# Kernel optimization log

Hardware: AMD Instinct MI355X
Metric: run time of the kernel (lower is better)

The kernel has to match this reference:

```python
import jax, jax.numpy as jnp
import numpy as np

LN_EPS = 1e-5  # torch.nn.LayerNorm default


def setup_inputs() -> dict:
    key = jax.random.key(0)
    k1, k2, k3 = jax.random.split(key, 3)
    B, N, F, D = 8, 2048, 128, 128
    A_hat = jax.random.uniform(k1, (B, N, N), dtype=jnp.float32)
    X = jax.random.normal(k2, (B, N, F), dtype=jnp.float32)
    W = jax.random.normal(k3, (D, F), dtype=jnp.float32) * (1.0 / np.sqrt(F))
    b = jnp.zeros((D,), dtype=jnp.float32)
    gamma = jnp.ones((D,), dtype=jnp.float32)
    beta = jnp.zeros((D,), dtype=jnp.float32)
    return {"A_hat": A_hat, "X": X, "W": W, "b": b, "gamma": gamma, "beta": beta}


def reference(A_hat, X, W, b, gamma, beta):
    # batched aggregation: H[b] = A_hat[b] @ X[b]   (torch loop over batch, vectorized here)
    H = jnp.einsum('bnm,bmf->bnf', A_hat, X)
    # linear: torch nn.Linear stores W as [out, in]
    H = jnp.einsum('bnf,df->bnd', H, W) + b
    # LayerNorm over last dim, then ReLU (dropout p=0 -> identity)
    mu = jnp.mean(H, axis=-1, keepdims=True)
    var = jnp.mean((H - mu) ** 2, axis=-1, keepdims=True)
    Hn = (H - mu) * jax.lax.rsqrt(var + LN_EPS) * gamma + beta
    return jax.nn.relu(Hn)
```

## Files before the change

### kernel.cpp

```cpp
#include <hip/hip_runtime.h>
#include <stdint.h>

#define B_DIM 8
#define N_DIM 2048
#define F_DIM 128
#define LN_EPS 1e-5f

typedef __attribute__((ext_vector_type(8))) short short8;
typedef __attribute__((ext_vector_type(4))) float floatx4;

__device__ __forceinline__ ushort f2bf(float f) {
    union { float f; uint32_t u; } c;
    c.f = f;
    uint32_t u = c.u;
    return (ushort)((u + 0x7FFFu + ((u >> 16) & 1u)) >> 16);
}

__device__ __forceinline__ uint32_t pk2bf(float a, float b) {
    union { float f; uint32_t u; } x, y;
    x.f = a; y.f = b;
    return ((x.u + 0x8000u) >> 16) | ((y.u + 0x8000u) & 0xFFFF0000u);
}

__device__ __forceinline__ short8 pack8(float4 lo, float4 hi) {
    union { uint32_t u[4]; short8 s; } r;
    r.u[0] = pk2bf(lo.x, lo.y);
    r.u[1] = pk2bf(lo.z, lo.w);
    r.u[2] = pk2bf(hi.x, hi.y);
    r.u[3] = pk2bf(hi.z, hi.w);
    return r.s;
}

__device__ __forceinline__ void load_lds16(const ushort* g, ushort* l) {
    __builtin_amdgcn_global_load_lds(
        (const __attribute__((address_space(1))) void*)g,
        (__attribute__((address_space(3))) void*)l,
        16, 0, 0);
}

__global__ __launch_bounds__(256) void k_prep(const float* __restrict__ X,
                                              const float* __restrict__ W,
                                              ushort* __restrict__ Yt) {
    __shared__ __align__(16) ushort Xs[64 * 128];
    const int t = threadIdx.x;
    const int lane = t & 63;
    const int w = t >> 6;
    const int q = lane >> 4;
    const int mr = lane & 15;

    const int b = blockIdx.x >> 5;
    const int k0 = (blockIdx.x & 31) * 64;

    const int r = t >> 2;
    const int f0 = (t & 3) * 32;
    const float* src = X + (((size_t)b * N_DIM) + k0 + r) * F_DIM + f0;
    float4 v[8];
#pragma unroll
    for (int p = 0; p < 8; ++p) v[p] = ((const float4*)src)[p];
#pragma unroll
    for (int c2 = 0; c2 < 4; ++c2) {
        int chunk = (f0 >> 3) + c2;
        *(short8*)(Xs + r * 128 + ((chunk ^ (r & 7)) * 8)) =
            pack8(v[2 * c2], v[2 * c2 + 1]);
    }
    __syncthreads();

    floatx4 acc[4][2];
#pragma unroll
    for (int i = 0; i < 4; ++i)
#pragma unroll
        for (int j = 0; j < 2; ++j) acc[i][j] = (floatx4){0.f, 0.f, 0.f, 0.f};

#pragma unroll
    for (int ks = 0; ks < 4; ++ks) {
        short8 af[4];
#pragma unroll
        for (int i = 0; i < 4; ++i) {
            int m = i * 16 + mr;
            af[i] = *(const short8*)(Xs + m * 128 + (((ks * 4 + q) ^ (m & 7)) * 8));
        }
#pragma unroll
        for (int j = 0; j < 2; ++j) {
            const float* wp = W + (w * 32 + j * 16 + mr) * F_DIM + ks * 32 + q * 8;
            short8 wb = pack8(((const float4*)wp)[0], ((const float4*)wp)[1]);
#pragma unroll
            for (int i = 0; i < 4; ++i)
                acc[i][j] = __builtin_amdgcn_mfma_f32_16x16x32_bf16(af[i], wb,
                                                                    acc[i][j], 0, 0, 0);
        }
    }

#pragma unroll
    for (int i = 0; i < 4; ++i)
#pragma unroll
        for (int j = 0; j < 2; ++j) {
            int d = w * 32 + j * 16 + mr;
            union { ushort s[4]; uint2 u; } o;
#pragma unroll
            for (int r2 = 0; r2 < 4; ++r2) o.s[r2] = f2bf(acc[i][j][r2]);
            *(uint2*)(Yt + (((size_t)b * F_DIM) + d) * N_DIM + k0 + i * 16 + q * 4) =
                o.u;
        }
}

__global__ __launch_bounds__(256, 2) void k_fused(const float* __restrict__ A,
                                                  const ushort* __restrict__ Yt,
                                                  const float* __restrict__ bias,
                                                  const float* __restrict__ gamma,
                                                  const float* __restrict__ beta,
                                                  float* __restrict__ out) {
    __shared__ __align__(16) char smem[81920];
    ushort* const As0 = (ushort*)smem;
    ushort* const As1 = (ushort*)(smem + 8192);
    ushort* const Bs0 = (ushort*)(smem + 16384);
    ushort* const Bs1 = (ushort*)(smem + 16384 + 32768);
    float (*const Pt)[132] = (float(*)[132])smem;

    const int t = threadIdx.x;
    const int lane = t & 63;
    const int w = t >> 6;
    const int q = lane >> 4;
    const int mr = lane & 15;

    const int bid = blockIdx.x;
    const int bb = bid & 7;
    const int m0 = (bid >> 3) * 32;

    const float* Ab = A + ((size_t)bb * N_DIM + m0) * N_DIM;
    const ushort* Yb = Yt + (size_t)bb * F_DIM * N_DIM;

    const int arow = t >> 3;
    const int asw_ = arow & 7;
    const float* a_src = Ab + (size_t)arow * N_DIM + (t & 7) * 16;
    const int a_off0 = arow * 128 + ((((t & 7) * 2) ^ asw_) * 8);
    const int a_off1 = arow * 128 + ((((t & 7) * 2 + 1) ^ asw_) * 8);

    const ushort* b_src[8];
    int b_off[8];
#pragma unroll
    for (int p = 0; p < 8; ++p) {
        int c = p * 256 + t;
        int n = c >> 4;
        int kc = (c & 15) ^ (n & 7);
        b_src[p] = Yb + (size_t)n * N_DIM + kc * 8;
        b_off[p] = c * 8;
    }

    floatx4 acc[2][2];
#pragma unroll
    for (int i = 0; i < 2; ++i)
#pragma unroll
        for (int j = 0; j < 2; ++j) acc[i][j] = (floatx4){0.f, 0.f, 0.f, 0.f};

    auto stageB = [&](int k0, ushort* Bn) {
#pragma unroll
        for (int p = 0; p < 8; ++p) load_lds16(b_src[p] + k0, Bn + b_off[p]);
    };
    auto packA = [&](float4 v0, float4 v1, float4 v2, float4 v3, ushort* An) {
        *(short8*)(An + a_off0) = pack8(v0, v1);
        *(short8*)(An + a_off1) = pack8(v2, v3);
    };
    auto compute = [&](const ushort* Ac, const ushort* Bc) {
#pragma unroll
        for (int ks = 0; ks < 4; ++ks) {
            short8 af[2], bfr[2];
#pragma unroll
            for (int i = 0; i < 2; ++i) {
                int m = mr + i * 16;
                af[i] = *(const short8*)(Ac + m * 128 + (((ks * 4 + q) ^ (m & 7)) * 8));
            }
#pragma unroll
            for (int j = 0; j < 2; ++j) {
                int n = w * 32 + j * 16 + mr;
                bfr[j] = *(const short8*)(Bc + n * 128 + (((ks * 4 + q) ^ (n & 7)) * 8));
            }
#pragma unroll
            for (int i = 0; i < 2; ++i)
#pragma unroll
                for (int j = 0; j < 2; ++j)
                    acc[i][j] = __builtin_amdgcn_mfma_f32_16x16x32_bf16(
                        af[i], bfr[j], acc[i][j], 0, 0, 0);
        }
    };

    float4 r0a, r0b, r0c, r0d, r1a, r1b, r1c, r1d;

    {
        const float4* ap = (const float4*)(a_src);
        r0a = ap[0]; r0b = ap[1]; r0c = ap[2]; r0d = ap[3];
        stageB(0, Bs0);
        packA(r0a, r0b, r0c, r0d, As0);
        __builtin_amdgcn_sched_barrier(0);
        const float4* ap1 = (const float4*)(a_src + 128);
        r1a = ap1[0]; r1b = ap1[1]; r1c = ap1[2]; r1d = ap1[3];
    }
    asm volatile("s_waitcnt vmcnt(4) lgkmcnt(0)" ::: "memory");
    __builtin_amdgcn_s_barrier();

#pragma unroll 1
    for (int tt = 0; tt < 14; tt += 2) {
        const int k0 = tt * 128;
        stageB(k0 + 128, Bs1);
        __builtin_amdgcn_sched_barrier(0);
        {
            const float4* ap = (const float4*)(a_src + k0 + 256);
            r0a = ap[0]; r0b = ap[1]; r0c = ap[2]; r0d = ap[3];
        }
        compute(As0, Bs0);
        packA(r1a, r1b, r1c, r1d, As1);
        asm volatile("s_waitcnt vmcnt(4) lgkmcnt(0)" ::: "memory");
        __builtin_amdgcn_s_barrier();

        stageB(k0 + 256, Bs0);
        __builtin_amdgcn_sched_barrier(0);
        {
            const float4* ap = (const float4*)(a_src + k0 + 384);
            r1a = ap[0]; r1b = ap[1]; r1c = ap[2]; r1d = ap[3];
        }
        compute(As1, Bs1);
        packA(r0a, r0b, r0c, r0d, As0);
        asm volatile("s_waitcnt vmcnt(4) lgkmcnt(0)" ::: "memory");
        __builtin_amdgcn_s_barrier();
    }

    stageB(15 * 128, Bs1);
    compute(As0, Bs0);
    packA(r1a, r1b, r1c, r1d, As1);
    asm volatile("s_waitcnt vmcnt(0) lgkmcnt(0)" ::: "memory");
    __builtin_amdgcn_s_barrier();

    compute(As1, Bs1);
    __syncthreads();

#pragma unroll
    for (int j = 0; j < 2; ++j) {
        int col = w * 32 + j * 16 + mr;
        float bcol = bias[col];
#pragma unroll
        for (int r = 0; r < 4; ++r) {
            Pt[q * 4 + r][col] = acc[0][j][r] + bcol;
            Pt[16 + q * 4 + r][col] = acc[1][j][r] + bcol;
        }
    }
    __syncthreads();

    const int row = t >> 3;
    const int seg = t & 7;
    float v[16];
    float s = 0.f, s2 = 0.f;
#pragma unroll
    for (int u = 0; u < 16; ++u) {
        v[u] = Pt[row][seg * 16 + u];
        s += v[u];
        s2 += v[u] * v[u];
    }
    s += __shfl_xor(s, 1);  s2 += __shfl_xor(s2, 1);
    s += __shfl_xor(s, 2);  s2 += __shfl_xor(s2, 2);
    s += __shfl_xor(s, 4);  s2 += __shfl_xor(s2, 4);
    float mu = s * (1.0f / 128.0f);
    float var = s2 * (1.0f / 128.0f) - mu * mu;
    float rs = rsqrtf(var + LN_EPS);

    float4 o[4];
    float* of = (float*)o;
#pragma unroll
    for (int u = 0; u < 16; ++u) {
        int d = seg * 16 + u;
        float y = (v[u] - mu) * rs * gamma[d] + beta[d];
        of[u] = fmaxf(y, 0.0f);
    }
    float4* dst = (float4*)(out + ((size_t)bb * N_DIM + m0 + row) * F_DIM + seg * 16);
    dst[0] = o[0]; dst[1] = o[1]; dst[2] = o[2]; dst[3] = o[3];
}

extern "C" void kernel_launch(void* const* d_in, const int* in_sizes, int n_in,
                              void* d_out, int out_size, void* d_ws, size_t ws_size,
                              hipStream_t stream) {
    const float* A     = (const float*)d_in[0];
    const float* X     = (const float*)d_in[1];
    const float* W     = (const float*)d_in[2];
    const float* bias  = (const float*)d_in[3];
    const float* gamma = (const float*)d_in[4];
    const float* beta  = (const float*)d_in[5];
    float* out = (float*)d_out;

    ushort* Yt = (ushort*)d_ws;

    k_prep<<<dim3(256), 256, 0, stream>>>(X, W, Yt);
    k_fused<<<dim3(512), 256, 0, stream>>>(A, Yt, bias, gamma, beta, out);
}
```

Before: 214.4 us.

## Load B fragments directly from global into registers instead of staging in LDS

Removes the LDS staging of the bf16 Yt (B operand) tiles via global_load_lds and has each wave load its own B MFMA fragments straight from global memory into double-buffered registers. LDS use drops from 80KB to 17KB, which could allow more resident blocks and removes LDS read traffic and bank pressure for B. The cost is higher register use, strided 16-byte global loads with no cross-wave sharing (each wave reads its own columns, so no redundancy across waves but less coalescing), and a pipeline that now relies on compiler-inserted vmcnt waits rather than explicit ones.

```diff
diff --git a/kernel.cpp b/kernel.cpp
--- a/kernel.cpp
+++ b/kernel.cpp
@@ -29,13 +29,6 @@
     r.u[2] = pk2bf(hi.x, hi.y);
     r.u[3] = pk2bf(hi.z, hi.w);
     return r.s;
-}
-
-__device__ __forceinline__ void load_lds16(const ushort* g, ushort* l) {
-    __builtin_amdgcn_global_load_lds(
-        (const __attribute__((address_space(1))) void*)g,
-        (__attribute__((address_space(3))) void*)l,
-        16, 0, 0);
 }
 
 __global__ __launch_bounds__(256) void k_prep(const float* __restrict__ X,
@@ -109,11 +102,9 @@
                                                   const float* __restrict__ gamma,
                                                   const float* __restrict__ beta,
                                                   float* __restrict__ out) {
-    __shared__ __align__(16) char smem[81920];
+    __shared__ __align__(16) char smem[17408];
     ushort* const As0 = (ushort*)smem;
     ushort* const As1 = (ushort*)(smem + 8192);
-    ushort* const Bs0 = (ushort*)(smem + 16384);
-    ushort* const Bs1 = (ushort*)(smem + 16384 + 32768);
     float (*const Pt)[132] = (float(*)[132])smem;
 
     const int t = threadIdx.x;
@@ -135,16 +126,7 @@
     const int a_off0 = arow * 128 + ((((t & 7) * 2) ^ asw_) * 8);
     const int a_off1 = arow * 128 + ((((t & 7) * 2 + 1) ^ asw_) * 8);
 
-    const ushort* b_src[8];
-    int b_off[8];
-#pragma unroll
-    for (int p = 0; p < 8; ++p) {
-        int c = p * 256 + t;
-        int n = c >> 4;
-        int kc = (c & 15) ^ (n & 7);
-        b_src[p] = Yb + (size_t)n * N_DIM + kc * 8;
-        b_off[p] = c * 8;
-    }
+    const ushort* b_base = Yb + (size_t)(w * 32 + mr) * N_DIM + q * 8;
 
     floatx4 acc[2][2];
 #pragma unroll
@@ -152,18 +134,29 @@
 #pragma unroll
         for (int j = 0; j < 2; ++j) acc[i][j] = (floatx4){0.f, 0.f, 0.f, 0.f};
 
-    auto stageB = [&](int k0, ushort* Bn) {
-#pragma unroll
-        for (int p = 0; p < 8; ++p) load_lds16(b_src[p] + k0, Bn + b_off[p]);
-    };
-    auto packA = [&](float4 v0, float4 v1, float4 v2, float4 v3, ushort* An) {
-        *(short8*)(An + a_off0) = pack8(v0, v1);
-        *(short8*)(An + a_off1) = pack8(v2, v3);
-    };
-    auto compute = [&](const ushort* Ac, const ushort* Bc) {
+    float4 r0[4], r1[4];
+    short8 B0[8], B1[8];
+
+    auto loadA = [&](int k0, float4* r) {
+        const float4* ap = (const float4*)(a_src + k0);
+        r[0] = ap[0]; r[1] = ap[1]; r[2] = ap[2]; r[3] = ap[3];
+    };
+    auto loadB = [&](int k0, short8* Bv) {
+#pragma unroll
+        for (int j = 0; j < 2; ++j)
+#pragma unroll
+            for (int ks = 0; ks < 4; ++ks)
+                Bv[j * 4 + ks] = *(const short8*)(b_base + (size_t)j * 16 * N_DIM +
+                                                  k0 + ks * 32);
+    };
+    auto packA = [&](const float4* r, ushort* An) {
+        *(short8*)(An + a_off0) = pack8(r[0], r[1]);
+        *(short8*)(An + a_off1) = pack8(r[2], r[3]);
+    };
+    auto compute = [&](const ushort* Ac, const short8* Bv) {
 #pragma unroll
         for (int ks = 0; ks < 4; ++ks) {
-            short8 af[2], bfr[2];
+            short8 af[2];
 #pragma unroll
             for (int i = 0; i < 2; ++i) {
                 int m = mr + i * 16;
@@ -171,65 +164,59 @@
             }
 #pragma unroll
             for (int j = 0; j < 2; ++j) {
-                int n = w * 32 + j * 16 + mr;
-                bfr[j] = *(const short8*)(Bc + n * 128 + (((ks * 4 + q) ^ (n & 7)) * 8));
+#pragma unroll
+                for (int i = 0; i < 2; ++i)
+                    acc[i][j] = __builtin_amdgcn_mfma_f32_16x16x32_bf16(
+                        af[i], Bv[j * 4 + ks], acc[i][j], 0, 0, 0);
             }
-#pragma unroll
-            for (int i = 0; i < 2; ++i)
-#pragma unroll
-                for (int j = 0; j < 2; ++j)
-                    acc[i][j] = __builtin_amdgcn_mfma_f32_16x16x32_bf16(
-                        af[i], bfr[j], acc[i][j], 0, 0, 0);
-        }
-    };
-
-    float4 r0a, r0b, r0c, r0d, r1a, r1b, r1c, r1d;
-
-    {
-        const float4* ap = (const float4*)(a_src);
-        r0a = ap[0]; r0b = ap[1]; r0c = ap[2]; r0d = ap[3];
-        stageB(0, Bs0);
-        packA(r0a, r0b, r0c, r0d, As0);
-        __builtin_amdgcn_sched_barrier(0);
-        const float4* ap1 = (const float4*)(a_src + 128);
-        r1a = ap1[0]; r1b = ap1[1]; r1c = ap1[2]; r1d = ap1[3];
-    }
-    asm volatile("s_waitcnt vmcnt(4) lgkmcnt(0)" ::: "memory");
+        }
+    };
+
+    loadA(0, r0);
+    loadB(0, B0);
+    packA(r0, As0);
+    loadA(128, r1);
+    loadB(128, B1);
+    asm volatile("s_waitcnt lgkmcnt(0)" ::: "memory");
     __builtin_amdgcn_s_barrier();
 
 #pragma unroll 1
-    for (int tt = 0; tt < 14; tt += 2) {
-        const int k0 = tt * 128;
-        stageB(k0 + 128, Bs1);
-        __builtin_amdgcn_sched_barrier(0);
-        {
-            const float4* ap = (const float4*)(a_src + k0 + 256);
-            r0a = ap[0]; r0b = ap[1]; r0c = ap[2]; r0d = ap[3];
-        }
-        compute(As0, Bs0);
-        packA(r1a, r1b, r1c, r1d, As1);
-        asm volatile("s_waitcnt vmcnt(4) lgkmcnt(0)" ::: "memory");
+    for (int tt = 0; tt < 12; tt += 2) {
+        compute(As0, B0);
+        loadB(tt * 128 + 256, B0);
+        loadA(tt * 128 + 256, r0);
+        packA(r1, As1);
+        asm volatile("s_waitcnt lgkmcnt(0)" ::: "memory");
         __builtin_amdgcn_s_barrier();
 
-        stageB(k0 + 256, Bs0);
-        __builtin_amdgcn_sched_barrier(0);
-        {
-            const float4* ap = (const float4*)(a_src + k0 + 384);
-            r1a = ap[0]; r1b = ap[1]; r1c = ap[2]; r1d = ap[3];
-        }
-        compute(As1, Bs1);
-        packA(r0a, r0b, r0c, r0d, As0);
-        asm volatile("s_waitcnt vmcnt(4) lgkmcnt(0)" ::: "memory");
+        compute(As1, B1);
+        loadB(tt * 128 + 384, B1);
+        loadA(tt * 128 + 384, r1);
+        packA(r0, As0);
+        asm volatile("s_waitcnt lgkmcnt(0)" ::: "memory");
         __builtin_amdgcn_s_barrier();
     }
 
-    stageB(15 * 128, Bs1);
-    compute(As0, Bs0);
-    packA(r1a, r1b, r1c, r1d, As1);
-    asm volatile("s_waitcnt vmcnt(0) lgkmcnt(0)" ::: "memory");
-    __builtin_amdgcn_s_barrier();
-
-    compute(As1, Bs1);
+    compute(As0, B0);
+    loadB(14 * 128, B0);
+    loadA(14 * 128, r0);
+    packA(r1, As1);
+    asm volatile("s_waitcnt lgkmcnt(0)" ::: "memory");
+    __builtin_amdgcn_s_barrier();
+
+    compute(As1, B1);
+    loadB(15 * 128, B1);
+    loadA(15 * 128, r1);
+    packA(r0, As0);
+    asm volatile("s_waitcnt lgkmcnt(0)" ::: "memory");
+    __builtin_amdgcn_s_barrier();
+
+    compute(As0, B0);
+    packA(r1, As1);
+    asm volatile("s_waitcnt lgkmcnt(0)" ::: "memory");
+    __builtin_amdgcn_s_barrier();
+
+    compute(As1, B1);
     __syncthreads();
 
 #pragma unroll
```

New measurement: 221.7 us. +3.4%, slower.
